# Kernel tuning notes

Measured on AMD Instinct MI355X. Metric: run time of the kernel, lower is better.

Reference implementation:

```python
import jax, jax.numpy as jnp
import numpy as np

B, S, D = 2, 2048, 1024
H, DK, DV = 16, 64, 64
DF = 4096
EPS = 1e-5


def _layer_norm(x, g, b):
    mu = jnp.mean(x, axis=-1, keepdims=True)
    var = jnp.mean((x - mu) ** 2, axis=-1, keepdims=True)
    return (x - mu) * jax.lax.rsqrt(var + EPS) * g + b


def setup_inputs() -> dict:
    key = jax.random.key(0)
    ks = jax.random.split(key, 12)
    s = lambda fan_in: 1.0 / np.sqrt(fan_in)
    return {
        "enc_input": jax.random.normal(ks[0], (B, S, D), dtype=jnp.float32),
        "wq": jax.random.uniform(ks[1], (D, H * DK), jnp.float32, -s(D), s(D)),
        "wk": jax.random.uniform(ks[2], (D, H * DK), jnp.float32, -s(D), s(D)),
        "wv": jax.random.uniform(ks[3], (D, H * DV), jnp.float32, -s(D), s(D)),
        "wo": jax.random.uniform(ks[4], (H * DV, D), jnp.float32, -s(H * DV), s(H * DV)),
        "w1": jax.random.uniform(ks[5], (D, DF), jnp.float32, -s(D), s(D)),
        "b1": jax.random.uniform(ks[6], (DF,), jnp.float32, -s(D), s(D)),
        "w2": jax.random.uniform(ks[7], (DF, D), jnp.float32, -s(DF), s(DF)),
        "b2": jax.random.uniform(ks[8], (D,), jnp.float32, -s(DF), s(DF)),
        "ln1_g": jnp.ones((D,), jnp.float32),
        "ln1_b": jnp.zeros((D,), jnp.float32),
        "ln2_g": jnp.ones((D,), jnp.float32),
        "ln2_b": jnp.zeros((D,), jnp.float32),
    }


def reference(enc_input, wq, wk, wv, wo, w1, b1, w2, b2, ln1_g, ln1_b, ln2_g, ln2_b):
    x = enc_input
    # QKV projections -> [B, H, S, d]
    q = (x @ wq).reshape(B, S, H, DK).transpose(0, 2, 1, 3)
    k = (x @ wk).reshape(B, S, H, DK).transpose(0, 2, 1, 3)
    v = (x @ wv).reshape(B, S, H, DV).transpose(0, 2, 1, 3)
    # scaled dot-product attention (scale = 1/sqrt(d_k), dropout is identity at eval)
    score = jnp.einsum("bhqd,bhkd->bhqk", q, k) / jnp.sqrt(jnp.float32(DK))
    attn = jax.nn.softmax(score, axis=-1)
    ctx = jnp.einsum("bhqk,bhkd->bhqd", attn, v)
    ctx = ctx.transpose(0, 2, 1, 3).reshape(B, S, H * DV)
    atn_out = ctx @ wo
    # Add & Norm 1
    h = _layer_norm(x + atn_out, ln1_g, ln1_b)
    # FFN
    ffn = jax.nn.relu(h @ w1 + b1) @ w2 + b2
    # Add & Norm 2
    return _layer_norm(h + ffn, ln2_g, ln2_b)
```

## Files before the change

### kernel.cpp

```cpp
#include <hip/hip_runtime.h>
#include <hip/hip_bf16.h>

typedef __bf16 bf16;
typedef __bf16 bf16x4 __attribute__((ext_vector_type(4)));
typedef __bf16 bf16x8 __attribute__((ext_vector_type(8)));
typedef float  f32x4  __attribute__((ext_vector_type(4)));

#define KB 2
#define KS 2048
#define KD 1024
#define KH 16
#define KM (KB*KS)
#define KQKVN 3072
#define KDF 4096

__device__ __forceinline__ f32x4 mfma16(bf16x8 a, bf16x8 b, f32x4 c) {
  return __builtin_amdgcn_mfma_f32_16x16x32_bf16(a, b, c, 0, 0, 0);
}

__device__ __forceinline__ void g2l16(const bf16* g, bf16* l) {
  __builtin_amdgcn_global_load_lds(
      (const __attribute__((address_space(1))) unsigned int*)g,
      (__attribute__((address_space(3))) unsigned int*)l, 16, 0, 0);
}

__global__ __launch_bounds__(256) void cvt_bf16_kernel(const float* __restrict__ in,
                                                       bf16* __restrict__ out, int n) {
  int i = (blockIdx.x * 256 + threadIdx.x) * 4;
  if (i >= n) return;
  f32x4 v = *reinterpret_cast<const f32x4*>(in + i);
  bf16x4 o;
  o[0] = (bf16)v[0]; o[1] = (bf16)v[1]; o[2] = (bf16)v[2]; o[3] = (bf16)v[3];
  *reinterpret_cast<bf16x4*>(out + i) = o;
}

__global__ __launch_bounds__(256) void wtrans_kernel(const float* __restrict__ W,
                                                     bf16* __restrict__ WT,
                                                     int K, int N) {
  __shared__ float tile[32][33];
  const int n0 = blockIdx.x * 32, k0 = blockIdx.y * 32;
  const int tx = threadIdx.x & 31, ty = threadIdx.x >> 5;
#pragma unroll
  for (int j = ty; j < 32; j += 8) tile[j][tx] = W[(size_t)(k0 + j) * N + n0 + tx];
  __syncthreads();
#pragma unroll
  for (int j = ty; j < 32; j += 8) WT[(size_t)(n0 + j) * K + k0 + tx] = (bf16)tile[tx][j];
}

__global__ __launch_bounds__(256) void kvpack_kernel(const bf16* __restrict__ qkv,
                                                     bf16* __restrict__ kp,
                                                     bf16* __restrict__ vt) {
  __shared__ bf16 tile[64][72];
  const int s0 = blockIdx.x * 64;
  const int bh = blockIdx.y;
  const int b = bh >> 4, h = bh & 15;
  const int t = threadIdx.x;
  const int r = t >> 3, c8 = (t & 7) * 8;
#pragma unroll
  for (int rr = r; rr < 64; rr += 32) {
    const size_t grow = (size_t)(b * KS + s0 + rr) * KQKVN + h * 64 + c8;
    bf16x8 kv = *reinterpret_cast<const bf16x8*>(&qkv[grow + 1024]);
    *reinterpret_cast<bf16x8*>(&kp[((size_t)bh * KS + s0 + rr) * 64 + c8]) = kv;
    bf16x8 vv = *reinterpret_cast<const bf16x8*>(&qkv[grow + 2048]);
#pragma unroll
    for (int j = 0; j < 8; j++) tile[rr][c8 + j] = vv[j];
  }
  __syncthreads();
#pragma unroll
  for (int dd = r; dd < 64; dd += 32) {
    bf16x8 v;
#pragma unroll
    for (int j = 0; j < 8; j++) v[j] = tile[c8 + j][dd];
    *reinterpret_cast<bf16x8*>(&vt[(size_t)bh * 64 * KS + (size_t)dd * KS + s0 + c8]) = v;
  }
}

struct P4 { bf16* p[4]; };

template <typename OUT_T, bool RELU, bool HAS_BIAS, bool SPLITK>
__global__ __launch_bounds__(512, 2) void gemm256(const bf16* __restrict__ A,
                                                  const bf16* __restrict__ BT,
                                                  OUT_T* __restrict__ C, P4 pr,
                                                  const float* __restrict__ bias,
                                                  int M, int N, int K, int Kslice) {
  extern __shared__ __align__(16) bf16 sm[];
  const int tid = threadIdx.x, lane = tid & 63, w = tid >> 6;
  const int wr = w >> 2, wc = w & 3;
  const int gx = gridDim.x;
  const int nwg = gx * gridDim.y;
  int flat = blockIdx.y * gx + blockIdx.x;
  flat = (flat & 7) * (nwg >> 3) + (flat >> 3);
  const int bn = (flat % gx) * 256;
  const int bm = (flat / gx) * 256;
  const int z = blockIdx.z;
  const int NT = (SPLITK ? Kslice : K) >> 5;
  const int lr = lane & 15, hi = lane >> 4;
  int srow[2], scol[2];
#pragma unroll
  for (int j = 0; j < 2; j++) {
    const int u = j * 512 + tid;
    srow[j] = u >> 2;
    scol[j] = (((u & 3) ^ ((u >> 2) & 3))) * 8;
  }
  const bf16* Abase = A + (size_t)bm * K + (SPLITK ? z * Kslice : 0);
  const bf16* Bbase = BT + (size_t)bn * K + (SPLITK ? z * Kslice : 0);
  auto stage = [&](int t) {
    bf16* dst = sm + (size_t)(t & 3) * 16384;
    const int k0 = t * 32;
#pragma unroll
    for (int j = 0; j < 2; j++) {
      g2l16(Abase + (size_t)srow[j] * K + k0 + scol[j], dst + (j * 512 + w * 64) * 8);
      g2l16(Bbase + (size_t)srow[j] * K + k0 + scol[j],
            dst + 8192 + (j * 512 + w * 64) * 8);
    }
  };
  f32x4 acc[8][4] = {};
  stage(0); stage(1); stage(2);
  for (int t = 0; t < NT; t++) {
    const int rem = NT - 1 - t;
    if (rem >= 2)      asm volatile("s_waitcnt vmcnt(8)" ::: "memory");
    else if (rem == 1) asm volatile("s_waitcnt vmcnt(4)" ::: "memory");
    else               asm volatile("s_waitcnt vmcnt(0)" ::: "memory");
    __builtin_amdgcn_sched_barrier(0);
    __builtin_amdgcn_s_barrier();
    __builtin_amdgcn_sched_barrier(0);
    if (t + 3 < NT) stage(t + 3);
    const bf16* sa = sm + (size_t)(t & 3) * 16384;
    const bf16* sb = sa + 8192;
    bf16x8 af[8], bfr[4];
#pragma unroll
    for (int mf = 0; mf < 8; mf++) {
      const int row = wr * 128 + mf * 16 + lr;
      af[mf] = *(const bf16x8*)&sa[row * 32 + ((hi ^ (row & 3)) * 8)];
    }
#pragma unroll
    for (int nf = 0; nf < 4; nf++) {
      const int row = wc * 64 + nf * 16 + lr;
      bfr[nf] = *(const bf16x8*)&sb[row * 32 + ((hi ^ (row & 3)) * 8)];
    }
    __builtin_amdgcn_s_setprio(1);
#pragma unroll
    for (int mf = 0; mf < 8; mf++)
#pragma unroll
      for (int nf = 0; nf < 4; nf++)
        acc[mf][nf] = mfma16(af[mf], bfr[nf], acc[mf][nf]);
    __builtin_amdgcn_s_setprio(0);
  }
  const int rg = hi * 4, cl = lr;
  if (SPLITK) {
    bf16* P = pr.p[z];
#pragma unroll
    for (int mf = 0; mf < 8; mf++)
#pragma unroll
      for (int nf = 0; nf < 4; nf++) {
        const int col = bn + wc * 64 + nf * 16 + cl;
#pragma unroll
        for (int i = 0; i < 4; i++) {
          const int row = bm + wr * 128 + mf * 16 + rg + i;
          P[(size_t)row * N + col] = (bf16)acc[mf][nf][i];
        }
      }
  } else {
#pragma unroll
    for (int mf = 0; mf < 8; mf++)
#pragma unroll
      for (int nf = 0; nf < 4; nf++) {
        const int col = bn + wc * 64 + nf * 16 + cl;
        float bv = 0.f;
        if (HAS_BIAS) bv = bias[col];
#pragma unroll
        for (int i = 0; i < 4; i++) {
          const int row = bm + wr * 128 + mf * 16 + rg + i;
          float v = acc[mf][nf][i] + bv;
          if (RELU) v = fmaxf(v, 0.f);
          C[(size_t)row * N + col] = (OUT_T)v;
        }
      }
  }
}

__global__ __launch_bounds__(256) void ffn2_reduce_kernel(const bf16* __restrict__ p0,
                                                          const bf16* __restrict__ p1,
                                                          const bf16* __restrict__ p2,
                                                          const bf16* __restrict__ p3,
                                                          const float* __restrict__ b2,
                                                          float* __restrict__ out) {
  const size_t i = ((size_t)blockIdx.x * 256 + threadIdx.x) * 8;
  bf16x8 a0 = *(const bf16x8*)(p0 + i);
  bf16x8 a1 = *(const bf16x8*)(p1 + i);
  bf16x8 a2 = *(const bf16x8*)(p2 + i);
  bf16x8 a3 = *(const bf16x8*)(p3 + i);
  const int col = (int)(i & (KD - 1));
  f32x4 b0 = *(const f32x4*)(b2 + col);
  f32x4 b1 = *(const f32x4*)(b2 + col + 4);
  f32x4 o0, o1;
#pragma unroll
  for (int j = 0; j < 4; j++)
    o0[j] = (float)a0[j] + (float)a1[j] + (float)a2[j] + (float)a3[j] + b0[j];
#pragma unroll
  for (int j = 0; j < 4; j++)
    o1[j] = (float)a0[j + 4] + (float)a1[j + 4] + (float)a2[j + 4] + (float)a3[j + 4] + b1[j];
  *(f32x4*)(out + i) = o0;
  *(f32x4*)(out + i + 4) = o1;
}

template <typename OUT_T, bool RELU, bool HAS_BIAS, int BN>
__global__ __launch_bounds__(256) void gemm_bt(const bf16* __restrict__ A,
                                               const bf16* __restrict__ BT,
                                               OUT_T* __restrict__ C,
                                               const float* __restrict__ bias,
                                               int M, int N, int K) {
  constexpr int NF = BN / 32;
  __shared__ __align__(16) bf16 sa[2][128 * 32];
  __shared__ __align__(16) bf16 sb[2][BN * 32];
  const int t = threadIdx.x, lane = t & 63, w = t >> 6;
  const int gx = gridDim.x;
  const int nwg = gx * gridDim.y;
  int flat = blockIdx.y * gx + blockIdx.x;
  if ((nwg & 7) == 0) flat = (flat & 7) * (nwg >> 3) + (flat >> 3);
  const int bn = (flat % gx) * BN;
  const int bm = (flat / gx) * 128;
  const int wr = w >> 1, wc = w & 1;
  const int wcol = wc * (BN / 2);
  const int lr = lane & 15, lk = (lane >> 4) * 8;
  const int srow = w * 16 + (lane >> 2);
  const int scol = (lane & 3) * 8;
  f32x4 acc[4][NF] = {};
  const int NT = K >> 5;
  auto stage = [&](int kt, int buf) {
#pragma unroll
    for (int i = 0; i < 2; i++)
      g2l16(A + (size_t)(bm + i * 64 + srow) * K + kt * 32 + scol,
            &sa[buf][(i * 64 + w * 16) * 32]);
#pragma unroll
    for (int i = 0; i < BN / 64; i++)
      g2l16(BT + (size_t)(bn + i * 64 + srow) * K + kt * 32 + scol,
            &sb[buf][(i * 64 + w * 16) * 32]);
  };
  stage(0, 0);
  int cur = 0;
  for (int kt = 0; kt < NT; kt++) {
    __syncthreads();
    if (kt + 1 < NT) stage(kt + 1, cur ^ 1);
    bf16x8 af[4], bfr[NF];
#pragma unroll
    for (int m = 0; m < 4; m++)
      af[m] = *(const bf16x8*)&sa[cur][(wr * 64 + m * 16 + lr) * 32 + lk];
#pragma unroll
    for (int n = 0; n < NF; n++)
      bfr[n] = *(const bf16x8*)&sb[cur][(wcol + n * 16 + lr) * 32 + lk];
#pragma unroll
    for (int m = 0; m < 4; m++)
#pragma unroll
      for (int n = 0; n < NF; n++)
        acc[m][n] = mfma16(af[m], bfr[n], acc[m][n]);
    cur ^= 1;
  }
  const int rg = (lane >> 4) * 4, cl = lane & 15;
#pragma unroll
  for (int m = 0; m < 4; m++)
#pragma unroll
    for (int n = 0; n < NF; n++) {
      const int col = bn + wcol + n * 16 + cl;
      float bv = 0.f;
      if (HAS_BIAS) bv = bias[col];
#pragma unroll
      for (int i = 0; i < 4; i++) {
        const int row = bm + wr * 64 + m * 16 + rg + i;
        float v = acc[m][n][i] + bv;
        if (RELU) v = fmaxf(v, 0.f);
        C[(size_t)row * N + col] = (OUT_T)v;
      }
    }
}

__global__ __launch_bounds__(256) void attn_kernel(const bf16* __restrict__ qkv,
                                                   const bf16* __restrict__ kp,
                                                   const bf16* __restrict__ vt,
                                                   bf16* __restrict__ ctx) {
  __shared__ __align__(16) bf16 ksm[2][64 * 64];
  __shared__ __align__(16) bf16 vsm[2][64 * 64];
  __shared__ __align__(16) bf16 psm[4][32 * 64];
  const int t = threadIdx.x, lane = t & 63, w = t >> 6;
  const int flat = blockIdx.y * 16 + blockIdx.x;
  const int xcd = flat & 7, jj = flat >> 3;
  const int bh = xcd + 8 * (jj >> 4);
  const int qb = jj & 15;
  const int b = bh >> 4, h = bh & 15;
  const int qbase = qb * 128 + w * 32;
  const int lr = lane & 15, hi = lane >> 4;
  const int lk = hi * 8, rg = hi * 4, cl = lr;

  bf16x8 aq[2][2];
#pragma unroll
  for (int m = 0; m < 2; m++)
#pragma unroll
    for (int kk = 0; kk < 2; kk++) {
      bf16x8 v = *reinterpret_cast<const bf16x8*>(
          &qkv[(size_t)(b * KS + qbase + m * 16 + lr) * KQKVN + h * 64 + kk * 32 + lk]);
#pragma unroll
      for (int e = 0; e < 8; e++) v[e] = (bf16)((float)v[e] * 0.125f);
      aq[m][kk] = v;
    }

  const bf16* kpb = kp + (size_t)bh * KS * 64;
  const bf16* vtb = vt + (size_t)bh * 64 * KS;

  auto stageKV = [&](int kt0, int buf) {
#pragma unroll
    for (int i = 0; i < 2; i++) {
      const int q = i * 4096 + w * 1024 + (lane << 4);
      const int row = q >> 7;
      const int slot = ((q >> 4) & 7) ^ (row & 7);
      g2l16(kpb + (size_t)(kt0 + row) * 64 + slot * 8,
            &ksm[buf][(i * 4096 + w * 1024) >> 1]);
      g2l16(vtb + (size_t)row * KS + kt0 + slot * 8,
            &vsm[buf][(i * 4096 + w * 1024) >> 1]);
    }
  };

  f32x4 accd[2][4] = {};
  float lsum[2][4] = {};

  stageKV(0, 0);
  int cur = 0;
  char* pb = (char*)&psm[w][0];
  for (int kt0 = 0; kt0 < KS; kt0 += 64) {
    __syncthreads();
    if (kt0 + 64 < KS) stageKV(kt0 + 64, cur ^ 1);
    const char* kb = (const char*)&ksm[cur][0];
    const char* vb = (const char*)&vsm[cur][0];
    bf16x8 bk[4][2];
#pragma unroll
    for (int n = 0; n < 4; n++)
#pragma unroll
      for (int kk = 0; kk < 2; kk++) {
        const int row = n * 16 + lr;
        bk[n][kk] = *(const bf16x8*)(kb + row * 128 +
                                     ((kk * 64 + hi * 16) ^ ((row & 7) << 4)));
      }
    f32x4 sc[2][4] = {};
#pragma unroll
    for (int m = 0; m < 2; m++)
#pragma unroll
      for (int n = 0; n < 4; n++)
#pragma unroll
        for (int kk = 0; kk < 2; kk++)
          sc[m][n] = mfma16(aq[m][kk], bk[n][kk], sc[m][n]);
#pragma unroll
    for (int m = 0; m < 2; m++)
#pragma unroll
      for (int n = 0; n < 4; n++)
#pragma unroll
        for (int i = 0; i < 4; i++) {
          const float p = __expf(sc[m][n][i]);
          lsum[m][i] += p;
          const int row = m * 16 + rg + i;
          *(bf16*)(pb + row * 128 + ((n * 32 + cl * 2) ^ ((row & 7) << 4))) = (bf16)p;
        }
    bf16x8 ap[2][2];
#pragma unroll
    for (int m = 0; m < 2; m++)
#pragma unroll
      for (int kk = 0; kk < 2; kk++) {
        const int row = m * 16 + lr;
        ap[m][kk] = *(const bf16x8*)(pb + row * 128 +
                                     ((kk * 64 + hi * 16) ^ ((row & 7) << 4)));
      }
    bf16x8 bv[4][2];
#pragma unroll
    for (int dt = 0; dt < 4; dt++)
#pragma unroll
      for (int kk = 0; kk < 2; kk++) {
        const int row = dt * 16 + lr;
        bv[dt][kk] = *(const bf16x8*)(vb + row * 128 +
                                      ((kk * 64 + hi * 16) ^ ((row & 7) << 4)));
      }
#pragma unroll
    for (int m = 0; m < 2; m++)
#pragma unroll
      for (int dt = 0; dt < 4; dt++)
#pragma unroll
        for (int kk = 0; kk < 2; kk++)
          accd[m][dt] = mfma16(ap[m][kk], bv[dt][kk], accd[m][dt]);
    cur ^= 1;
  }
  float rs_[2][4];
#pragma unroll
  for (int m = 0; m < 2; m++)
#pragma unroll
    for (int i = 0; i < 4; i++) {
      float s = lsum[m][i];
#pragma unroll
      for (int off = 1; off < 16; off <<= 1) s += __shfl_xor(s, off, 64);
      rs_[m][i] = 1.0f / s;
    }
#pragma unroll
  for (int m = 0; m < 2; m++)
#pragma unroll
    for (int dt = 0; dt < 4; dt++)
#pragma unroll
      for (int i = 0; i < 4; i++)
        ctx[(size_t)(b * KS + qbase + m * 16 + rg + i) * KD + h * 64 + dt * 16 + cl] =
            (bf16)(accd[m][dt][i] * rs_[m][i]);
}

template <bool ABF, bool OBF>
__global__ __launch_bounds__(256) void ln_kernel(const void* __restrict__ aptr,
                                                 const float* __restrict__ bsum,
                                                 const float* __restrict__ g,
                                                 const float* __restrict__ bet,
                                                 void* __restrict__ outp) {
  const int row = blockIdx.x;
  const int t = threadIdx.x;
  const int lane = t & 63, wid = t >> 6;
  float v[4];
  {
    f32x4 bv = *reinterpret_cast<const f32x4*>(&bsum[(size_t)row * KD + t * 4]);
    if (ABF) {
      bf16x4 av = *reinterpret_cast<const bf16x4*>(
          (const bf16*)aptr + (size_t)row * KD + t * 4);
#pragma unroll
      for (int j = 0; j < 4; j++) v[j] = (float)av[j] + bv[j];
    } else {
      f32x4 av = *reinterpret_cast<const f32x4*>(
          (const float*)aptr + (size_t)row * KD + t * 4);
#pragma unroll
      for (int j = 0; j < 4; j++) v[j] = av[j] + bv[j];
    }
  }
  float s = 0.f, s2 = 0.f;
#pragma unroll
  for (int j = 0; j < 4; j++) { s += v[j]; s2 += v[j] * v[j]; }
#pragma unroll
  for (int off = 32; off; off >>= 1) {
    s += __shfl_xor(s, off, 64);
    s2 += __shfl_xor(s2, off, 64);
  }
  __shared__ float red[8];
  if (lane == 0) { red[wid] = s; red[wid + 4] = s2; }
  __syncthreads();
  s = red[0] + red[1] + red[2] + red[3];
  s2 = red[4] + red[5] + red[6] + red[7];
  const float mu = s * (1.f / KD);
  const float var = s2 * (1.f / KD) - mu * mu;
  const float rs = rsqrtf(var + 1e-5f);
  if (OBF) {
    bf16x4 o;
#pragma unroll
    for (int j = 0; j < 4; j++)
      o[j] = (bf16)((v[j] - mu) * rs * g[t * 4 + j] + bet[t * 4 + j]);
    *reinterpret_cast<bf16x4*>((bf16*)outp + (size_t)row * KD + t * 4) = o;
  } else {
    f32x4 o;
#pragma unroll
    for (int j = 0; j < 4; j++)
      o[j] = (v[j] - mu) * rs * g[t * 4 + j] + bet[t * 4 + j];
    *reinterpret_cast<f32x4*>((float*)outp + (size_t)row * KD + t * 4) = o;
  }
}

extern "C" void kernel_launch(void* const* d_in, const int* in_sizes, int n_in,
                              void* d_out, int out_size, void* d_ws, size_t ws_size,
                              hipStream_t stream) {
  const float* x     = (const float*)d_in[0];
  const float* wq    = (const float*)d_in[1];
  const float* wk    = (const float*)d_in[2];
  const float* wv    = (const float*)d_in[3];
  const float* wo    = (const float*)d_in[4];
  const float* w1    = (const float*)d_in[5];
  const float* b1    = (const float*)d_in[6];
  const float* w2    = (const float*)d_in[7];
  const float* b2    = (const float*)d_in[8];
  const float* ln1g  = (const float*)d_in[9];
  const float* ln1b  = (const float*)d_in[10];
  const float* ln2g  = (const float*)d_in[11];
  const float* ln2b  = (const float*)d_in[12];
  float* out = (float*)d_out;

  char* ws = (char*)d_ws;
  bf16*  x_bf   = (bf16*)(ws + 0);
  bf16*  wqkvT  = (bf16*)(ws + 8388608);
  bf16*  woT    = (bf16*)(ws + 14680064);
  bf16*  w1T    = (bf16*)(ws + 16777216);
  bf16*  w2T    = (bf16*)(ws + 25165824);
  bf16*  qkv    = (bf16*)(ws + 33554432);
  bf16*  kp     = (bf16*)(ws + 58720256);
  bf16*  vt     = (bf16*)(ws + 67108864);
  float* proj   = (float*)(ws + 75497472);
  bf16*  ctx    = x_bf;
  bf16*  h_bf   = (bf16*)(ws + 8388608);
  bf16*  ffn1   = qkv;
  float* ffn2   = (float*)(ws + 33554432);
  P4 pr;
  pr.p[0] = (bf16*)(ws + 0);
  pr.p[1] = (bf16*)(ws + 16777216);
  pr.p[2] = (bf16*)(ws + 67108864);
  pr.p[3] = (bf16*)(ws + 75497472);
  P4 pzero = {};

  cvt_bf16_kernel<<<dim3(KM * KD / 1024), 256, 0, stream>>>(x, x_bf, KM * KD);
  wtrans_kernel<<<dim3(32, 32), 256, 0, stream>>>(wq, wqkvT, KD, KD);
  wtrans_kernel<<<dim3(32, 32), 256, 0, stream>>>(wk, wqkvT + 1024 * 1024, KD, KD);
  wtrans_kernel<<<dim3(32, 32), 256, 0, stream>>>(wv, wqkvT + 2048 * 1024, KD, KD);
  wtrans_kernel<<<dim3(32, 32), 256, 0, stream>>>(wo, woT, KD, KD);
  wtrans_kernel<<<dim3(128, 32), 256, 0, stream>>>(w1, w1T, KD, KDF);
  wtrans_kernel<<<dim3(32, 128), 256, 0, stream>>>(w2, w2T, KDF, KD);

  gemm256<bf16, false, false, false>
      <<<dim3(KQKVN / 256, KM / 256, 1), 512, 131072, stream>>>(
      x_bf, wqkvT, qkv, pzero, nullptr, KM, KQKVN, KD, KD);

  kvpack_kernel<<<dim3(KS / 64, KB * KH), 256, 0, stream>>>(qkv, kp, vt);

  attn_kernel<<<dim3(KS / 128, KB * KH), 256, 0, stream>>>(qkv, kp, vt, ctx);

  gemm_bt<float, false, false, 64><<<dim3(KD / 64, KM / 128), 256, 0, stream>>>(
      ctx, woT, proj, nullptr, KM, KD, KD);

  ln_kernel<false, true><<<dim3(KM), 256, 0, stream>>>(x, proj, ln1g, ln1b, h_bf);

  gemm256<bf16, true, true, false>
      <<<dim3(KDF / 256, KM / 256, 1), 512, 131072, stream>>>(
      h_bf, w1T, ffn1, pzero, b1, KM, KDF, KD, KD);

  gemm256<bf16, false, false, true>
      <<<dim3(KD / 256, KM / 256, 4), 512, 131072, stream>>>(
      ffn1, w2T, (bf16*)nullptr, pr, nullptr, KM, KD, KDF, KDF / 4);

  ffn2_reduce_kernel<<<dim3(KM * KD / 8 / 256), 256, 0, stream>>>(
      pr.p[0], pr.p[1], pr.p[2], pr.p[3], b2, ffn2);

  ln_kernel<true, false><<<dim3(KM), 256, 0, stream>>>(h_bf, ffn2, ln2g, ln2b, out);
}
```

Measured before the change: 257.5 us.

## Deepen attention K/V pipeline to four stages and vectorize P stores

The attention kernel's K/V shared-memory ring grows from two to four buffers, prefetching three tiles ahead with explicit vmcnt waits and a raw barrier in place of __syncthreads. Each thread now packs its four probability values into one bf16x4 LDS store instead of four scalar stores. To keep P@V correct under that packing, the V transpose kernel permutes the key order along the sequence. MFMA sections are wrapped in s_setprio. The extra K/V buffers double their LDS use, which may lower occupancy, and the hand-written vmcnt counts must exactly match the number of loads issued per stage.

```diff
diff --git a/kernel.cpp b/kernel.cpp
--- a/kernel.cpp
+++ b/kernel.cpp
@@ -70,7 +70,10 @@
   for (int dd = r; dd < 64; dd += 32) {
     bf16x8 v;
 #pragma unroll
-    for (int j = 0; j < 8; j++) v[j] = tile[c8 + j][dd];
+    for (int j = 0; j < 8; j++) {
+      const int pi = c8 + j;
+      v[j] = tile[((pi & 3) << 4) + (pi >> 2)][dd];
+    }
     *reinterpret_cast<bf16x8*>(&vt[(size_t)bh * 64 * KS + (size_t)dd * KS + s0 + c8]) = v;
   }
 }
@@ -278,8 +281,8 @@
                                                    const bf16* __restrict__ kp,
                                                    const bf16* __restrict__ vt,
                                                    bf16* __restrict__ ctx) {
-  __shared__ __align__(16) bf16 ksm[2][64 * 64];
-  __shared__ __align__(16) bf16 vsm[2][64 * 64];
+  __shared__ __align__(16) bf16 ksm[4][64 * 64];
+  __shared__ __align__(16) bf16 vsm[4][64 * 64];
   __shared__ __align__(16) bf16 psm[4][32 * 64];
   const int t = threadIdx.x, lane = t & 63, w = t >> 6;
   const int flat = blockIdx.y * 16 + blockIdx.x;
@@ -306,30 +309,37 @@
   const bf16* kpb = kp + (size_t)bh * KS * 64;
   const bf16* vtb = vt + (size_t)bh * 64 * KS;
 
-  auto stageKV = [&](int kt0, int buf) {
+  auto stageKV = [&](int tt) {
+    const int kt0 = tt * 64;
+    bf16* kd = &ksm[tt & 3][0];
+    bf16* vd = &vsm[tt & 3][0];
 #pragma unroll
     for (int i = 0; i < 2; i++) {
       const int q = i * 4096 + w * 1024 + (lane << 4);
       const int row = q >> 7;
       const int slot = ((q >> 4) & 7) ^ (row & 7);
-      g2l16(kpb + (size_t)(kt0 + row) * 64 + slot * 8,
-            &ksm[buf][(i * 4096 + w * 1024) >> 1]);
-      g2l16(vtb + (size_t)row * KS + kt0 + slot * 8,
-            &vsm[buf][(i * 4096 + w * 1024) >> 1]);
+      g2l16(kpb + (size_t)(kt0 + row) * 64 + slot * 8, kd + ((i * 4096 + w * 1024) >> 1));
+      g2l16(vtb + (size_t)row * KS + kt0 + slot * 8,   vd + ((i * 4096 + w * 1024) >> 1));
     }
   };
 
   f32x4 accd[2][4] = {};
   float lsum[2][4] = {};
 
-  stageKV(0, 0);
-  int cur = 0;
+  stageKV(0); stageKV(1); stageKV(2);
   char* pb = (char*)&psm[w][0];
-  for (int kt0 = 0; kt0 < KS; kt0 += 64) {
-    __syncthreads();
-    if (kt0 + 64 < KS) stageKV(kt0 + 64, cur ^ 1);
-    const char* kb = (const char*)&ksm[cur][0];
-    const char* vb = (const char*)&vsm[cur][0];
+  const int NT = KS / 64;
+  for (int tt = 0; tt < NT; tt++) {
+    const int rem = NT - 1 - tt;
+    if (rem >= 2)      asm volatile("s_waitcnt vmcnt(8)" ::: "memory");
+    else if (rem == 1) asm volatile("s_waitcnt vmcnt(4)" ::: "memory");
+    else               asm volatile("s_waitcnt vmcnt(0)" ::: "memory");
+    __builtin_amdgcn_sched_barrier(0);
+    __builtin_amdgcn_s_barrier();
+    __builtin_amdgcn_sched_barrier(0);
+    if (tt + 3 < NT) stageKV(tt + 3);
+    const char* kb = (const char*)&ksm[tt & 3][0];
+    const char* vb = (const char*)&vsm[tt & 3][0];
     bf16x8 bk[4][2];
 #pragma unroll
     for (int n = 0; n < 4; n++)
@@ -340,6 +350,7 @@
                                      ((kk * 64 + hi * 16) ^ ((row & 7) << 4)));
       }
     f32x4 sc[2][4] = {};
+    __builtin_amdgcn_s_setprio(1);
 #pragma unroll
     for (int m = 0; m < 2; m++)
 #pragma unroll
@@ -347,17 +358,21 @@
 #pragma unroll
         for (int kk = 0; kk < 2; kk++)
           sc[m][n] = mfma16(aq[m][kk], bk[n][kk], sc[m][n]);
+    __builtin_amdgcn_s_setprio(0);
 #pragma unroll
     for (int m = 0; m < 2; m++)
 #pragma unroll
-      for (int n = 0; n < 4; n++)
-#pragma unroll
-        for (int i = 0; i < 4; i++) {
+      for (int i = 0; i < 4; i++) {
+        bf16x4 pk;
+#pragma unroll
+        for (int n = 0; n < 4; n++) {
           const float p = __expf(sc[m][n][i]);
           lsum[m][i] += p;
-          const int row = m * 16 + rg + i;
-          *(bf16*)(pb + row * 128 + ((n * 32 + cl * 2) ^ ((row & 7) << 4))) = (bf16)p;
+          pk[n] = (bf16)p;
         }
+        const int row = m * 16 + rg + i;
+        *(bf16x4*)(pb + row * 128 + ((cl * 8) ^ ((row & 7) << 4))) = pk;
+      }
     bf16x8 ap[2][2];
 #pragma unroll
     for (int m = 0; m < 2; m++)
@@ -376,6 +391,7 @@
         bv[dt][kk] = *(const bf16x8*)(vb + row * 128 +
                                       ((kk * 64 + hi * 16) ^ ((row & 7) << 4)));
       }
+    __builtin_amdgcn_s_setprio(1);
 #pragma unroll
     for (int m = 0; m < 2; m++)
 #pragma unroll
@@ -383,7 +399,7 @@
 #pragma unroll
         for (int kk = 0; kk < 2; kk++)
           accd[m][dt] = mfma16(ap[m][kk], bv[dt][kk], accd[m][dt]);
-    cur ^= 1;
+    __builtin_amdgcn_s_setprio(0);
   }
   float rs_[2][4];
 #pragma unroll
```

Result: faster. 250.2 us (-2.8%).
